# Kernel optimization log

Hardware: AMD Instinct MI355X
Metric: run time of the kernel (lower is better)

## Reference

```python
import jax, jax.numpy as jnp
import numpy as np

KS = 11
SIGMA = 1.5

def _gaussian_kernel(ks=KS, sigma=SIGMA, dtype=jnp.float32):
    ax = jnp.arange(ks, dtype=dtype) - (ks - 1) / 2.0
    xx, yy = jnp.meshgrid(ax, ax, indexing='ij')
    k = jnp.exp(-(xx**2 + yy**2) / (2.0 * sigma * sigma))
    k = k / k.sum()
    return k[None, None, :, :]  # [1,1,ks,ks] (OIHW)

def _conv(x, w):
    pad = KS // 2
    return jax.lax.conv_general_dilated(
        x, w, window_strides=(1, 1), padding=[(pad, pad), (pad, pad)],
        dimension_numbers=('NCHW', 'OIHW', 'NCHW'))

def setup_inputs() -> dict:
    key = jax.random.key(0)
    kx, ky = jax.random.split(key)
    B, H, W = 64, 512, 512
    x = jax.random.uniform(kx, (B, 1, H, W), dtype=jnp.float32)
    y = jax.random.uniform(ky, (B, 1, H, W), dtype=jnp.float32)
    return {"x": x, "y": y}

def reference(x, y):
    w = _gaussian_kernel(dtype=x.dtype)
    mu_x = _conv(x, w)
    mu_y = _conv(y, w)
    mu_x2, mu_y2 = mu_x * mu_x, mu_y * mu_y
    mu_xy = mu_x * mu_y
    sigma_x2 = _conv(x * x, w) - mu_x2
    sigma_y2 = _conv(y * y, w) - mu_y2
    sigma_xy = _conv(x * y, w) - mu_xy
    C1 = 0.01 ** 2
    C2 = 0.03 ** 2
    ssim_map = (2 * mu_xy + C1) * (2 * sigma_xy + C2) / (
        (mu_x2 + mu_y2 + C1) * (sigma_x2 + sigma_y2 + C2) + 1e-12)
    return 1.0 - ssim_map.mean()
```

## Files before the change

### kernel.cpp

```cpp
#include <hip/hip_runtime.h>
#include <math.h>


typedef float v2f __attribute__((ext_vector_type(2)));

#define TSY  32
#define HR   42
#define RAWS 52
#define GX   16
#define GY   16
#define NPART (64 * GY * GX)

struct W11 { float w[11]; };

__global__ __launch_bounds__(256, 4) void ssim_main(
    const float* __restrict__ x, const float* __restrict__ y,
    float* __restrict__ partial, W11 wk, int atomic_mode)
{
    __shared__ __align__(16) float raw[2][HR][RAWS];
    __shared__ __align__(16) v2f hst[4][16 * HR];
    __shared__ float red[4];

    const int tid = threadIdx.x;
    const int bx = blockIdx.x, by = blockIdx.y, bz = blockIdx.z;
    const float* __restrict__ xb = x + (size_t)bz * (512 * 512);
    const float* __restrict__ yb = y + (size_t)bz * (512 * 512);
    const int ox = bx * 32;
    const int oy = by * TSY;

    const int NT1 = 2 * HR * 12;
    #pragma unroll
    for (int it = 0; it < 4; ++it) {
        const int i = tid + (it << 8);
        if (i < NT1) {
            const int a   = (i >= HR * 12) ? 1 : 0;
            const int j   = i - a * (HR * 12);
            const int row = j / 12;
            const int f4c = j - row * 12;
            const int gr  = oy - 5 + row;
            const int gc  = ox - 8 + (f4c << 2);
            const float* __restrict__ sb = a ? yb : xb;
            float4 v = {0.f, 0.f, 0.f, 0.f};
            if ((unsigned)gr < 512u) {
                const float* __restrict__ rp = sb + gr * 512;
                if ((unsigned)gc <= 508u) {
                    v = *(const float4*)(rp + gc);
                } else {
                    float e[4];
                    #pragma unroll
                    for (int t = 0; t < 4; ++t) {
                        const int c = gc + t;
                        e[t] = ((unsigned)c < 512u) ? rp[c] : 0.f;
                    }
                    v = make_float4(e[0], e[1], e[2], e[3]);
                }
            }
            *(float4*)&raw[a][row][f4c << 2] = v;
        }
    }
    __syncthreads();

    if (tid < HR * 4) {
        const int r = tid >> 2;
        const int g = tid & 3;
        const float4* __restrict__ px = (const float4*)&raw[0][r][g << 2];
        const float4* __restrict__ py = (const float4*)&raw[1][r][g << 2];
        float4 X[9], Y[9];
        #pragma unroll
        for (int k = 0; k < 9; ++k) X[k] = px[k];
        #pragma unroll
        for (int k = 0; k < 9; ++k) Y[k] = py[k];
        float fx[36], fy[36];
        #pragma unroll
        for (int k = 0; k < 9; ++k) {
            fx[4*k+0] = X[k].x; fx[4*k+1] = X[k].y;
            fx[4*k+2] = X[k].z; fx[4*k+3] = X[k].w;
            fy[4*k+0] = Y[k].x; fy[4*k+1] = Y[k].y;
            fy[4*k+2] = Y[k].z; fy[4*k+3] = Y[k].w;
        }

        v2f acc[4][4];
        #pragma unroll
        for (int q = 0; q < 4; ++q)
            #pragma unroll
            for (int oc = 0; oc < 4; ++oc) acc[q][oc] = (v2f)0.f;

        #pragma unroll
        for (int k = 0; k < 14; ++k) {
            const v2f xv = (v2f){fx[3 + k], fx[19 + k]};
            const v2f yv = (v2f){fy[3 + k], fy[19 + k]};
            const v2f ss = xv * xv + yv * yv;
            const v2f xy = xv * yv;
            #pragma unroll
            for (int oc = 0; oc < 4; ++oc) {
                const int j = k - oc;
                if (j < 0 || j > 10) continue;
                const float wj = wk.w[j];
                acc[0][oc] += wj * xv;
                acc[1][oc] += wj * yv;
                acc[2][oc] += wj * ss;
                acc[3][oc] += wj * xy;
            }
        }
        #pragma unroll
        for (int q = 0; q < 4; ++q)
            #pragma unroll
            for (int oc = 0; oc < 4; ++oc)
                hst[q][((g << 2) + oc) * HR + r] = acc[q][oc];
    }
    __syncthreads();

    float lsum = 0.f;
    if (tid < 128) {
        const int cp = tid & 15;
        const int m0 = (tid >> 4) << 2;
        v2f s[4][4];
        #pragma unroll
        for (int q = 0; q < 4; ++q) {
            const float4* __restrict__ p4 = (const float4*)&hst[q][cp * HR + m0];
            float4 Q[7];
            #pragma unroll
            for (int k = 0; k < 7; ++k) Q[k] = p4[k];
            #pragma unroll
            for (int o = 0; o < 4; ++o) {
                v2f a = (v2f)0.f;
                #pragma unroll
                for (int j = 0; j < 11; ++j) {
                    const int t = o + j;
                    const v2f rv = (t & 1) ? (v2f){Q[t >> 1].z, Q[t >> 1].w}
                                           : (v2f){Q[t >> 1].x, Q[t >> 1].y};
                    a += wk.w[j] * rv;
                }
                s[q][o] = a;
            }
        }

        const float C1 = 1e-4f, C2 = 9e-4f;
        #pragma unroll
        for (int o = 0; o < 4; ++o) {
            const v2f mx = s[0][o], my = s[1][o];
            const v2f mx2 = mx * mx, my2 = my * my, mxy = mx * my;
            const v2f sig_sum = s[2][o] - mx2 - my2;
            const v2f sig_xy  = s[3][o] - mxy;
            const v2f num = (2.f * mxy + C1) * (2.f * sig_xy + C2);
            const v2f den = (mx2 + my2 + C1) * (sig_sum + C2) + 1e-12f;
            lsum += num.x * __builtin_amdgcn_rcpf(den.x)
                  + num.y * __builtin_amdgcn_rcpf(den.y);
        }
    }

    #pragma unroll
    for (int off = 32; off; off >>= 1) lsum += __shfl_down(lsum, off);
    if ((tid & 63) == 0) red[tid >> 6] = lsum;
    __syncthreads();
    if (tid == 0) {
        const float v = red[0] + red[1] + red[2] + red[3];
        if (atomic_mode) atomicAdd(partial, v);
        else partial[(bz * GY + by) * GX + bx] = v;
    }
}

__global__ __launch_bounds__(1024) void ssim_fin(const float* __restrict__ partial,
                                                 float* __restrict__ out, int n)
{
    float s = 0.f;
    for (int i = threadIdx.x; i < n; i += 1024) s += partial[i];
    #pragma unroll
    for (int off = 32; off; off >>= 1) s += __shfl_down(s, off);
    __shared__ float red[16];
    if ((threadIdx.x & 63) == 0) red[threadIdx.x >> 6] = s;
    __syncthreads();
    if (threadIdx.x == 0) {
        float v = 0.f;
        #pragma unroll
        for (int i = 0; i < 16; ++i) v += red[i];
        out[0] = 1.0f - v * (1.0f / 16777216.0f);
    }
}

extern "C" void kernel_launch(void* const* d_in, const int* in_sizes, int n_in,
                              void* d_out, int out_size, void* d_ws, size_t ws_size,
                              hipStream_t stream) {
    const float* x = (const float*)d_in[0];
    const float* y = (const float*)d_in[1];
    float* out = (float*)d_out;
    float* ws  = (float*)d_ws;

    W11 wk;
    double e[11], s = 0.0;
    for (int i = 0; i < 11; ++i) {
        double d = (double)i - 5.0;
        e[i] = exp(-(d * d) / 4.5);
        s += e[i];
    }
    for (int i = 0; i < 11; ++i) wk.w[i] = (float)(e[i] / s);

    const bool use_partial = ws_size >= (size_t)NPART * sizeof(float);
    if (!use_partial) hipMemsetAsync(d_ws, 0, sizeof(float), stream);

    hipLaunchKernelGGL(ssim_main, dim3(GX, GY, 64), dim3(256), 0, stream,
                       x, y, ws, wk, use_partial ? 0 : 1);
    hipLaunchKernelGGL(ssim_fin, dim3(1), dim3(1024), 0, stream,
                       ws, out, use_partial ? NPART : 1);
}
```

Baseline: 236.7 us.

## Double tile height, alias LDS buffers, and swizzle block order

```diff
diff --git a/kernel.cpp b/kernel.cpp
--- a/kernel.cpp
+++ b/kernel.cpp
@@ -4,11 +4,11 @@
 
 typedef float v2f __attribute__((ext_vector_type(2)));
 
-#define TSY  32
-#define HR   42
-#define RAWS 52
+#define TSY  64
+#define HR   74
+#define RAWS 48
 #define GX   16
-#define GY   16
+#define GY   8
 #define NPART (64 * GY * GX)
 
 struct W11 { float w[11]; };
@@ -17,24 +17,24 @@
     const float* __restrict__ x, const float* __restrict__ y,
     float* __restrict__ partial, W11 wk, int atomic_mode)
 {
-    __shared__ __align__(16) float raw[2][HR][RAWS];
-    __shared__ __align__(16) v2f hst[4][16 * HR];
+    __shared__ __align__(16) float lds[9472];
     __shared__ float red[4];
 
     const int tid = threadIdx.x;
-    const int bx = blockIdx.x, by = blockIdx.y, bz = blockIdx.z;
+    const int lin = (int)blockIdx.x + GX * ((int)blockIdx.y + GY * (int)blockIdx.z);
+    const int swz = ((lin & 7) << 10) | (lin >> 3);
+    const int bx = swz & 15, by = (swz >> 4) & 7, bz = swz >> 7;
     const float* __restrict__ xb = x + (size_t)bz * (512 * 512);
     const float* __restrict__ yb = y + (size_t)bz * (512 * 512);
     const int ox = bx * 32;
     const int oy = by * TSY;
 
-    const int NT1 = 2 * HR * 12;
     #pragma unroll
-    for (int it = 0; it < 4; ++it) {
+    for (int it = 0; it < 7; ++it) {
         const int i = tid + (it << 8);
-        if (i < NT1) {
-            const int a   = (i >= HR * 12) ? 1 : 0;
-            const int j   = i - a * (HR * 12);
+        if (i < 1776) {
+            const int a   = (i >= 888) ? 1 : 0;
+            const int j   = i - a * 888;
             const int row = j / 12;
             const int f4c = j - row * 12;
             const int gr  = oy - 5 + row;
@@ -55,69 +55,89 @@
                     v = make_float4(e[0], e[1], e[2], e[3]);
                 }
             }
-            *(float4*)&raw[a][row][f4c << 2] = v;
-        }
-    }
-    __syncthreads();
-
-    if (tid < HR * 4) {
-        const int r = tid >> 2;
-        const int g = tid & 3;
-        const float4* __restrict__ px = (const float4*)&raw[0][r][g << 2];
-        const float4* __restrict__ py = (const float4*)&raw[1][r][g << 2];
-        float4 X[9], Y[9];
-        #pragma unroll
-        for (int k = 0; k < 9; ++k) X[k] = px[k];
-        #pragma unroll
-        for (int k = 0; k < 9; ++k) Y[k] = py[k];
-        float fx[36], fy[36];
-        #pragma unroll
-        for (int k = 0; k < 9; ++k) {
-            fx[4*k+0] = X[k].x; fx[4*k+1] = X[k].y;
-            fx[4*k+2] = X[k].z; fx[4*k+3] = X[k].w;
-            fy[4*k+0] = Y[k].x; fy[4*k+1] = Y[k].y;
-            fy[4*k+2] = Y[k].z; fy[4*k+3] = Y[k].w;
-        }
-
-        v2f acc[4][4];
+            ((float4*)lds)[i] = v;
+        }
+    }
+    __syncthreads();
+
+#define HCONV(T, ACC)                                                        \
+    {                                                                        \
+        const int r_ = (T) >> 2;                                             \
+        const int g_ = (T) & 3;                                              \
+        const float4* __restrict__ px = (const float4*)(lds + r_ * RAWS + (g_ << 2)); \
+        const float4* __restrict__ py = (const float4*)(lds + 3552 + r_ * RAWS + (g_ << 2)); \
+        float4 X[9], Y[9];                                                   \
+        _Pragma("unroll")                                                    \
+        for (int k = 0; k < 9; ++k) X[k] = px[k];                            \
+        _Pragma("unroll")                                                    \
+        for (int k = 0; k < 9; ++k) Y[k] = py[k];                            \
+        float fx[36], fy[36];                                                \
+        _Pragma("unroll")                                                    \
+        for (int k = 0; k < 9; ++k) {                                        \
+            fx[4*k+0] = X[k].x; fx[4*k+1] = X[k].y;                          \
+            fx[4*k+2] = X[k].z; fx[4*k+3] = X[k].w;                          \
+            fy[4*k+0] = Y[k].x; fy[4*k+1] = Y[k].y;                          \
+            fy[4*k+2] = Y[k].z; fy[4*k+3] = Y[k].w;                          \
+        }                                                                    \
+        _Pragma("unroll")                                                    \
+        for (int q = 0; q < 4; ++q)                                          \
+            _Pragma("unroll")                                                \
+            for (int oc = 0; oc < 4; ++oc) ACC[q][oc] = (v2f)0.f;            \
+        _Pragma("unroll")                                                    \
+        for (int k = 0; k < 14; ++k) {                                       \
+            const v2f xv = (v2f){fx[3 + k], fx[19 + k]};                     \
+            const v2f yv = (v2f){fy[3 + k], fy[19 + k]};                     \
+            const v2f ss = xv * xv + yv * yv;                                \
+            const v2f xy = xv * yv;                                          \
+            _Pragma("unroll")                                                \
+            for (int oc = 0; oc < 4; ++oc) {                                 \
+                const int j = k - oc;                      \
+                if (j < 0 || j > 10) continue;                               \
+                const float wj = wk.w[j];                                    \
+                ACC[0][oc] += wj * xv;                                       \
+                ACC[1][oc] += wj * yv;                                       \
+                ACC[2][oc] += wj * ss;                                       \
+                ACC[3][oc] += wj * xy;                                       \
+            }                                                                \
+        }                                                                    \
+    }
+
+    v2f accA[4][4], accB[4][4];
+    HCONV(tid, accA)
+    const bool hasB = (tid < 40);
+    if (hasB) { HCONV(256 + tid, accB) }
+    __syncthreads();
+
+    {
+        v2f* __restrict__ hst = (v2f*)lds;
+        const int rA = tid >> 2, gA = tid & 3;
         #pragma unroll
         for (int q = 0; q < 4; ++q)
             #pragma unroll
-            for (int oc = 0; oc < 4; ++oc) acc[q][oc] = (v2f)0.f;
-
-        #pragma unroll
-        for (int k = 0; k < 14; ++k) {
-            const v2f xv = (v2f){fx[3 + k], fx[19 + k]};
-            const v2f yv = (v2f){fy[3 + k], fy[19 + k]};
-            const v2f ss = xv * xv + yv * yv;
-            const v2f xy = xv * yv;
-            #pragma unroll
-            for (int oc = 0; oc < 4; ++oc) {
-                const int j = k - oc;
-                if (j < 0 || j > 10) continue;
-                const float wj = wk.w[j];
-                acc[0][oc] += wj * xv;
-                acc[1][oc] += wj * yv;
-                acc[2][oc] += wj * ss;
-                acc[3][oc] += wj * xy;
-            }
-        }
-        #pragma unroll
-        for (int q = 0; q < 4; ++q)
-            #pragma unroll
             for (int oc = 0; oc < 4; ++oc)
-                hst[q][((g << 2) + oc) * HR + r] = acc[q][oc];
-    }
-    __syncthreads();
-
+                hst[q * 1184 + (((gA << 2) + oc)) * HR + rA] = accA[q][oc];
+        if (hasB) {
+            const int t2 = 256 + tid;
+            const int rB = t2 >> 2, gB = t2 & 3;
+            #pragma unroll
+            for (int q = 0; q < 4; ++q)
+                #pragma unroll
+                for (int oc = 0; oc < 4; ++oc)
+                    hst[q * 1184 + (((gB << 2) + oc)) * HR + rB] = accB[q][oc];
+        }
+    }
+    __syncthreads();
+#undef HCONV
+
+    const int cp = tid & 15;
+    const int m0 = (tid >> 4) << 2;
     float lsum = 0.f;
-    if (tid < 128) {
-        const int cp = tid & 15;
-        const int m0 = (tid >> 4) << 2;
+    {
+        const v2f* __restrict__ hst = (const v2f*)lds;
         v2f s[4][4];
         #pragma unroll
         for (int q = 0; q < 4; ++q) {
-            const float4* __restrict__ p4 = (const float4*)&hst[q][cp * HR + m0];
+            const float4* __restrict__ p4 = (const float4*)(hst + q * 1184 + cp * HR + m0);
             float4 Q[7];
             #pragma unroll
             for (int k = 0; k < 7; ++k) Q[k] = p4[k];
```

After: 232.8 us. No clear change (-1.7%).
